# Performance work log

Hardware: AMD Instinct MI355X
Metric: run time of the kernel (lower is better)

Reference implementation:

```python
import jax, jax.numpy as jnp
import numpy as np

NHEAD = 8
TOPKS = (8, 8)  # topk per level, coarse -> fine


def _to_bshd(x):
    # [B, C, H, W] -> [B, H*W, nhead, d]  (matches rearrange 'b c h w -> b (h w) c' + view)
    b, c, h, w = x.shape
    return jnp.transpose(x.reshape(b, c, h * w), (0, 2, 1)).reshape(b, h * w, NHEAD, c // NHEAD)


def _coarse_level(q, k, v, topk):
    b, c, h, w = k.shape
    d = c // NHEAD
    q_, k_, v_ = _to_bshd(q), _to_bshd(k), _to_bshd(v)
    temp = 1.0 / (d ** 0.5)
    A = jax.nn.softmax(jnp.einsum('nlhd,nshd->nlsh', q_, k_) * temp, axis=2)  # [b,L,S,h]
    _, idx = jax.lax.top_k(jnp.swapaxes(A, 2, 3), topk)  # [b,L,h,k]
    idx = jnp.swapaxes(idx, 2, 3)                        # [b,L,k,h]
    msg = jnp.einsum('nlsh,nshd->nlhd', A, v_)           # [b,L,h,d]
    topk_pos = jnp.stack([idx // w, idx % w])            # [2,b,L,k,h]
    return msg, topk_pos


def _fine_level(q, k, v, topk_pos, topk_prev, topk):
    b, c, h0, w0 = q.shape
    w1 = k.shape[3]
    d = c // NHEAD
    k_, v_ = _to_bshd(k), _to_bshd(v)
    H2, W2 = h0 // 2, w0 // 2
    L0 = H2 * W2
    # query grouped into 2x2 quads: [b, L0, 4, h, d]
    q_ = q.reshape(b, c, H2, 2, W2, 2).transpose(0, 2, 4, 3, 5, 1).reshape(b, L0, 4, NHEAD, d)
    tp = topk_pos * 2  # coarse positions -> fine grid
    cand = [(tp[0] + x) * w1 + tp[1] + y for x in (0, 1) for y in (0, 1)]
    t2 = topk_prev * 4
    idx = jnp.stack(cand, axis=3).reshape(b, L0, t2, NHEAD)  # [b,L,t2,h]
    idx_bh = idx.transpose(0, 3, 1, 2).reshape(b, NHEAD, L0 * t2)

    def gather(p):  # p: [b,S,h,d] -> gathered [b,L,t2,h,d]
        g = jnp.take_along_axis(jnp.swapaxes(p, 1, 2), idx_bh[..., None], axis=2)
        return g.reshape(b, NHEAD, L0, t2, d).transpose(0, 2, 3, 1, 4)

    tk, tv = gather(k_), gather(v_)
    temp = 1.0 / (d ** 0.5)
    A = jax.nn.softmax(jnp.einsum('blqhd,blthd->blqth', q_, tk) * temp, axis=3)  # [b,L,4,t2,h]
    _, ti = jax.lax.top_k(jnp.moveaxis(A, 3, 4), topk)  # [b,L,4,h,k]
    ti = jnp.moveaxis(ti, 4, 3)                         # [b,L,4,k,h]
    msg = jnp.einsum('blqth,blthd->blqhd', A, tv)       # [b,L,4,h,d]
    idx_b = jnp.broadcast_to(idx[:, :, None], (b, L0, 4, t2, NHEAD))
    gidx = jnp.take_along_axis(idx_b, ti, axis=3)       # [b,L,4,k,h] flat fine-grid indices
    gidx = gidx.reshape(b, H2, W2, 2, 2, topk, NHEAD).transpose(0, 1, 3, 2, 4, 5, 6)
    gidx = gidx.reshape(b, h0 * w0, topk, NHEAD)
    return msg, gidx


def _forward(q_fine, q_coarse, k_fine, k_coarse, v_fine, v_coarse, weight):
    msg0, topk_pos = _coarse_level(q_coarse, k_coarse, v_coarse, TOPKS[0])
    msg1, _ = _fine_level(q_fine, k_fine, v_fine, topk_pos, TOPKS[0], TOPKS[1])
    w = jax.nn.softmax(weight, axis=0)
    fm = msg0 * w[0]                  # [b,Lc,h,d]
    fm = fm[:, :, None] + msg1 * w[1]  # [b,Lc,4,h,d]
    b, Hc, Wc = q_coarse.shape[0], q_coarse.shape[2], q_coarse.shape[3]
    d = fm.shape[-1]
    # rearrange 'b (H W) (t1 t2) h d -> b (H t1 W t2) h d'
    fm = fm.reshape(b, Hc, Wc, 2, 2, NHEAD, d).transpose(0, 1, 3, 2, 4, 5, 6)
    return fm.reshape(b, Hc * Wc * 4, NHEAD, d)


def setup_inputs() -> dict:
    key = jax.random.key(0)
    ks = jax.random.split(key, 7)
    B, C = 4, 128
    return {
        'q_fine': jax.random.normal(ks[0], (B, C, 64, 64), jnp.float32),
        'q_coarse': jax.random.normal(ks[1], (B, C, 32, 32), jnp.float32),
        'k_fine': jax.random.normal(ks[2], (B, C, 64, 64), jnp.float32),
        'k_coarse': jax.random.normal(ks[3], (B, C, 32, 32), jnp.float32),
        'v_fine': jax.random.normal(ks[4], (B, C, 64, 64), jnp.float32),
        'v_coarse': jax.random.normal(ks[5], (B, C, 32, 32), jnp.float32),
        'weight': jax.random.normal(ks[6], (2,), jnp.float32),
    }


def reference(q_fine, q_coarse, k_fine, k_coarse, v_fine, v_coarse, weight):
    return _forward(q_fine, q_coarse, k_fine, k_coarse, v_fine, v_coarse, weight)
```

## Files before the change

kernel.cpp:

```cpp
#include <hip/hip_runtime.h>
#include <stdint.h>

#define TEMP 0.25f

typedef unsigned short u16;
typedef short v8s __attribute__((ext_vector_type(8)));
typedef float v4f __attribute__((ext_vector_type(4)));

static __device__ __forceinline__ uint32_t f2b_bits(float f){
    union { float f; uint32_t i; } x; x.f = f;
    uint32_t u = x.i;
    return (u + 0x7FFFu + ((u >> 16) & 1u)) >> 16;
}
static __device__ __forceinline__ float b2f(u16 u){
    union { uint32_t i; float f; } x; x.i = ((uint32_t)u) << 16; return x.f;
}
static __device__ __forceinline__ float bl(uint32_t u){
    union { uint32_t i; float f; } x; x.i = u << 16; return x.f;
}
static __device__ __forceinline__ float bh(uint32_t u){
    union { uint32_t i; float f; } x; x.i = u & 0xffff0000u; return x.f;
}
static __device__ __forceinline__ uint4 pack8(const uint32_t* e){
    return make_uint4(e[0] | (e[1] << 16), e[2] | (e[3] << 16),
                      e[4] | (e[5] << 16), e[6] | (e[7] << 16));
}
union U8S { uint4 u; v8s s; };
union I4S { int i[4]; v8s s; };
static __device__ __forceinline__ v8s asv8s(uint4 u){ U8S x; x.u = u; return x.s; }
static __device__ __forceinline__ v8s swapq(v8s v){
    union { v8s s; int i[4]; } x; x.s = v;
    #pragma unroll
    for (int k = 0; k < 4; ++k) x.i[k] = __shfl_xor(x.i[k], 32);
    return x.s;
}

__global__ __launch_bounds__(256)
void pack_coarse(const float* __restrict__ kc, const float* __restrict__ vc,
                 uint4* __restrict__ KP1, uint4* __restrict__ KP3,
                 uint4* __restrict__ VP1)
{
    const int bh = blockIdx.x;
    const int kv = blockIdx.y;
    const int z  = blockIdx.z;
    const int b = bh >> 3, h = bh & 7;
    const int tid = threadIdx.x;
    const size_t sbase = (size_t)(b * 128 + h * 16) * 1024;
    const size_t fbase = (size_t)bh * 64 * 64;

    #pragma unroll
    for (int it = 0; it < 2; ++it){
        int task = it * 256 + tid;
        int kt = z * 8 + (task >> 6), ln = task & 63;
        int quad = ln >> 4, col = ln & 15;
        if (kv == 0){
            uint32_t e1[8], e3[8];
            #pragma unroll
            for (int j = 0; j < 8; ++j){
                int dch = (quad & 1) * 8 + j;
                float x = kc[sbase + (size_t)dch * 1024 + kt * 16 + col];
                uint32_t u0 = f2b_bits(x);
                float r1 = x - b2f((u16)u0);
                uint32_t u1 = f2b_bits(r1);
                float r2 = r1 - b2f((u16)u1);
                uint32_t u2 = f2b_bits(r2);
                e1[j] = (quad < 2) ? u0 : u1;
                e3[j] = (quad < 2) ? u2 : u0;
            }
            KP1[fbase + kt * 64 + ln] = pack8(e1);
            KP3[fbase + kt * 64 + ln] = pack8(e3);
        } else {
            uint32_t e[8];
            #pragma unroll
            for (int j = 0; j < 8; ++j){
                int key = kt * 16 + (quad & 1) * 8 + j;
                float x = vc[sbase + (size_t)col * 1024 + key];
                uint32_t u0 = f2b_bits(x);
                uint32_t u1 = f2b_bits(x - b2f((u16)u0));
                e[j] = (quad < 2) ? u0 : u1;
            }
            VP1[fbase + kt * 64 + ln] = pack8(e);
        }
    }
}

__global__ __launch_bounds__(256)
void coarse_mfma(const float* __restrict__ qc,
                 const uint4* __restrict__ KP1, const uint4* __restrict__ KP3,
                 const uint4* __restrict__ VP1,
                 float* __restrict__ msg0, int* __restrict__ topk_out)
{
    const int ltile = blockIdx.x;
    const int h = blockIdx.y, b = blockIdx.z;
    const int bh = b * 8 + h;
    const int tid = threadIdx.x, lane = tid & 63, wv = tid >> 6;
    const int quad = lane >> 4, col = lane & 15;
    const int lbase = ltile * 16;

    __shared__ uint32_t tls[4][16 * 20];
    __shared__ float rred[2][4][16];
    __shared__ float pvred[4][16][16];
    __shared__ float tkv[4][16][8];
    __shared__ int   tki[4][16][8];

    v8s a1, a3;
    {
        int row = lbase + col;
        int dch0 = (quad & 1) * 8;
        #pragma unroll
        for (int j = 0; j < 8; ++j){
            float x = qc[(size_t)(b * 128 + h * 16 + dch0 + j) * 1024 + row] * TEMP;
            uint32_t u0 = f2b_bits(x);
            float r1 = x - b2f((u16)u0);
            uint32_t u1 = f2b_bits(r1);
            float r2 = r1 - b2f((u16)u1);
            uint32_t u2 = f2b_bits(r2);
            a1[j] = (short)(quad < 2 ? u0 : u1);
            a3[j] = (short)(quad < 2 ? u0 : u2);
        }
    }

    const size_t fbase = (size_t)bh * 64 * 64;
    v4f sc[16];
    #pragma unroll
    for (int kt = 0; kt < 16; ++kt){
        int ktg = wv * 16 + kt;
        v8s b1 = asv8s(KP1[fbase + (size_t)ktg * 64 + lane]);
        v8s b3 = asv8s(KP3[fbase + (size_t)ktg * 64 + lane]);
        v8s b2 = swapq(b1);
        v4f c = {0.f, 0.f, 0.f, 0.f};
        c = __builtin_amdgcn_mfma_f32_16x16x32_bf16(a1, b1, c, 0, 0, 0);
        c = __builtin_amdgcn_mfma_f32_16x16x32_bf16(a1, b2, c, 0, 0, 0);
        c = __builtin_amdgcn_mfma_f32_16x16x32_bf16(a3, b3, c, 0, 0, 0);
        sc[kt] = c;
    }

    #pragma unroll
    for (int r = 0; r < 4; ++r){
        float m = sc[0][r];
        #pragma unroll
        for (int kt = 1; kt < 16; ++kt) m = fmaxf(m, sc[kt][r]);
        #pragma unroll
        for (int off = 1; off < 16; off <<= 1) m = fmaxf(m, __shfl_xor(m, off));
        if (col == 0) rred[0][wv][quad * 4 + r] = m;
    }
    __syncthreads();
    #pragma unroll
    for (int r = 0; r < 4; ++r){
        int row = quad * 4 + r;
        float m = fmaxf(fmaxf(rred[0][0][row], rred[0][1][row]),
                        fmaxf(rred[0][2][row], rred[0][3][row]));
        #pragma unroll
        for (int kt = 0; kt < 16; ++kt) sc[kt][r] = __expf(sc[kt][r] - m);
    }
    #pragma unroll
    for (int r = 0; r < 4; ++r){
        float s = 0.f;
        #pragma unroll
        for (int kt = 0; kt < 16; ++kt) s += sc[kt][r];
        #pragma unroll
        for (int off = 1; off < 16; off <<= 1) s += __shfl_xor(s, off);
        if (col == 0) rred[1][wv][quad * 4 + r] = s;
    }

    v4f acc = {0.f, 0.f, 0.f, 0.f};
    uint32_t* tw = tls[wv];
    const int rdbase = col * 20 + 8 * (quad & 1);
    const uint32_t selp = (quad < 2) ? 0x05040100u : 0x07060302u;
    #pragma unroll
    for (int kt = 0; kt < 16; ++kt){
        #pragma unroll
        for (int r = 0; r < 4; ++r){
            float x = sc[kt][r];
            uint32_t u0 = f2b_bits(x);
            uint32_t u1 = f2b_bits(x - b2f((u16)u0));
            tw[(quad * 4 + r) * 20 + col] = u0 | (u1 << 16);
        }
        __builtin_amdgcn_s_waitcnt(0xC07F);
        uint4 d0 = *(const uint4*)&tw[rdbase];
        uint4 d1 = *(const uint4*)&tw[rdbase + 4];
        I4S ux;
        ux.i[0] = __builtin_amdgcn_perm(d0.y, d0.x, selp);
        ux.i[1] = __builtin_amdgcn_perm(d0.w, d0.z, selp);
        ux.i[2] = __builtin_amdgcn_perm(d1.y, d1.x, selp);
        ux.i[3] = __builtin_amdgcn_perm(d1.w, d1.z, selp);
        v8s ap = ux.s;
        v8s bv1 = asv8s(VP1[fbase + (size_t)(wv * 16 + kt) * 64 + lane]);
        v8s bv2 = swapq(bv1);
        acc = __builtin_amdgcn_mfma_f32_16x16x32_bf16(ap, bv1, acc, 0, 0, 0);
        acc = __builtin_amdgcn_mfma_f32_16x16x32_bf16(ap, bv2, acc, 0, 0, 0);
    }
    #pragma unroll
    for (int r = 0; r < 4; ++r) pvred[wv][quad * 4 + r][col] = acc[r];

    #pragma unroll
    for (int r = 0; r < 4; ++r){
        int row = quad * 4 + r;
        #pragma unroll
        for (int rnd = 0; rnd < 8; ++rnd){
            float bv = sc[0][r]; int bk = 0;
            #pragma unroll
            for (int kt = 1; kt < 16; ++kt){
                bool g = sc[kt][r] > bv;
                bv = g ? sc[kt][r] : bv; bk = g ? kt : bk;
            }
            int bi = bk * 16 + col;
            #pragma unroll
            for (int off = 1; off < 16; off <<= 1){
                float ov = __shfl_xor(bv, off);
                int   oi = __shfl_xor(bi, off);
                bool g = (ov > bv) || (ov == bv && oi < bi);
                bv = g ? ov : bv; bi = g ? oi : bi;
            }
            if ((bi & 15) == col){
                int ktw = bi >> 4;
                #pragma unroll
                for (int kt = 0; kt < 16; ++kt)
                    if (kt == ktw) sc[kt][r] = -1.0f;
            }
            if (col == rnd){ tkv[wv][row][rnd] = bv; tki[wv][row][rnd] = wv * 256 + bi; }
        }
    }
    __syncthreads();

    {
        int row = tid >> 4, dd = tid & 15;
        float v = pvred[0][row][dd] + pvred[1][row][dd] +
                  pvred[2][row][dd] + pvred[3][row][dd];
        float s = rred[1][0][row] + rred[1][1][row] +
                  rred[1][2][row] + rred[1][3][row];
        msg0[((size_t)((b * 1024 + lbase + row) * 8 + h)) * 16 + dd] = v / s;
    }
    if (tid < 16){
        int row = tid;
        int* tp = topk_out + (((b * 1024 + lbase + row) * 8 + h) * 8);
        int p[4] = {0, 0, 0, 0};
        #pragma unroll
        for (int rnd = 0; rnd < 8; ++rnd){
            float bv = -3.0f; int bw = 0, bi = 0x7fffffff;
            #pragma unroll
            for (int w = 0; w < 4; ++w){
                float v = tkv[w][row][p[w]];
                int   i = tki[w][row][p[w]];
                bool g = (v > bv) || (v == bv && i < bi);
                bv = g ? v : bv; bi = g ? i : bi; bw = g ? w : bw;
            }
            tp[rnd] = bi;
            p[bw]++;
        }
    }
}

__global__ __launch_bounds__(512, 2)
void coarse_kernel(const float* __restrict__ qc, const float* __restrict__ kc,
                   const float* __restrict__ vc, float* __restrict__ msg0,
                   int* __restrict__ topk_out)
{
    const int ltile = blockIdx.x;
    const int h = blockIdx.y, b = blockIdx.z;
    const int tid = threadIdx.x;
    const int lane = tid & 63, wv = tid >> 6;
    const int lbase = ltile * 32;
    __shared__ float sKV[16 * 1024];
    const size_t base = (size_t)(b * 128 + h * 16) * 1024;
    {
        const float4* gK = (const float4*)(kc + base);
        float4* lK = (float4*)sKV;
        #pragma unroll
        for (int i = 0; i < 8; ++i) lK[tid + 512 * i] = gK[tid + 512 * i];
    }
    float qreg[4];
    {
        int dq = lane & 15;
        #pragma unroll
        for (int li = 0; li < 4; ++li){
            int l = lbase + wv * 4 + li;
            qreg[li] = qc[base + (size_t)dq * 1024 + l] * TEMP;
        }
    }
    __syncthreads();
    float p[4][16];
    #pragma unroll
    for (int li = 0; li < 4; ++li)
        #pragma unroll
        for (int j = 0; j < 16; ++j) p[li][j] = 0.f;
    #pragma unroll
    for (int dch = 0; dch < 16; ++dch){
        float kf[16];
        #pragma unroll
        for (int ch = 0; ch < 4; ++ch){
            float4 kv = *(const float4*)&sKV[dch * 1024 + ch * 256 + (lane << 2)];
            kf[ch*4+0] = kv.x; kf[ch*4+1] = kv.y; kf[ch*4+2] = kv.z; kf[ch*4+3] = kv.w;
        }
        float qs[4];
        #pragma unroll
        for (int li = 0; li < 4; ++li) qs[li] = __shfl(qreg[li], dch);
        #pragma unroll
        for (int li = 0; li < 4; ++li)
            #pragma unroll
            for (int j = 0; j < 16; ++j) p[li][j] = fmaf(qs[li], kf[j], p[li][j]);
    }
    float invs[4];
    #pragma unroll
    for (int li = 0; li < 4; ++li){
        float m = p[li][0];
        #pragma unroll
        for (int j = 1; j < 16; ++j) m = fmaxf(m, p[li][j]);
        #pragma unroll
        for (int off = 32; off > 0; off >>= 1) m = fmaxf(m, __shfl_xor(m, off));
        float s = 0.f;
        #pragma unroll
        for (int j = 0; j < 16; ++j){ p[li][j] = __expf(p[li][j] - m); s += p[li][j]; }
        #pragma unroll
        for (int off = 32; off > 0; off >>= 1) s += __shfl_xor(s, off);
        invs[li] = 1.0f / s;
    }
    __syncthreads();
    {
        const float4* gV = (const float4*)(vc + base);
        float4* lV = (float4*)sKV;
        #pragma unroll
        for (int i = 0; i < 8; ++i) lV[tid + 512 * i] = gV[tid + 512 * i];
    }
    __syncthreads();
    float outv = 0.f;
    #pragma unroll
    for (int dd = 0; dd < 16; ++dd){
        float vf[16];
        #pragma unroll
        for (int ch = 0; ch < 4; ++ch){
            float4 vv = *(const float4*)&sKV[dd * 1024 + ch * 256 + (lane << 2)];
            vf[ch*4+0] = vv.x; vf[ch*4+1] = vv.y; vf[ch*4+2] = vv.z; vf[ch*4+3] = vv.w;
        }
        float a[4];
        #pragma unroll
        for (int li = 0; li < 4; ++li){
            float s = 0.f;
            #pragma unroll
            for (int j = 0; j < 16; ++j) s = fmaf(p[li][j], vf[j], s);
            a[li] = s;
        }
        #pragma unroll
        for (int off = 32; off > 0; off >>= 1)
            #pragma unroll
            for (int li = 0; li < 4; ++li) a[li] += __shfl_xor(a[li], off);
        #pragma unroll
        for (int li = 0; li < 4; ++li)
            outv = (lane == li * 16 + dd) ? a[li] * invs[li] : outv;
    }
    {
        int li = lane >> 4, dd = lane & 15;
        int l = lbase + wv * 4 + li;
        msg0[(size_t)((b * 1024 + l) * 8 + h) * 16 + dd] = outv;
    }
    const int lanebase = lane << 4;
    int mytk = 0;
    for (int r = 0; r < 8; ++r){
        float bv[4]; int bi[4];
        #pragma unroll
        for (int li = 0; li < 4; ++li){
            float v0[8]; int j0[8];
            #pragma unroll
            for (int k = 0; k < 8; ++k){
                bool g = p[li][2*k+1] > p[li][2*k];
                v0[k] = g ? p[li][2*k+1] : p[li][2*k];
                j0[k] = g ? 2*k+1 : 2*k;
            }
            float v1[4]; int j1[4];
            #pragma unroll
            for (int k = 0; k < 4; ++k){
                bool g = v0[2*k+1] > v0[2*k];
                v1[k] = g ? v0[2*k+1] : v0[2*k];
                j1[k] = g ? j0[2*k+1] : j0[2*k];
            }
            float v2[2]; int j2[2];
            #pragma unroll
            for (int k = 0; k < 2; ++k){
                bool g = v1[2*k+1] > v1[2*k];
                v2[k] = g ? v1[2*k+1] : v1[2*k];
                j2[k] = g ? j1[2*k+1] : j1[2*k];
            }
            bool g3 = v2[1] > v2[0];
            bv[li] = g3 ? v2[1] : v2[0];
            bi[li] = lanebase | (g3 ? j2[1] : j2[0]);
        }
        #pragma unroll
        for (int off = 32; off > 0; off >>= 1){
            #pragma unroll
            for (int li = 0; li < 4; ++li){
                float ov = __shfl_xor(bv[li], off);
                int   oi = __shfl_xor(bi[li], off);
                bool g = (ov > bv[li]) || (ov == bv[li] && oi < bi[li]);
                bv[li] = g ? ov : bv[li];
                bi[li] = g ? oi : bi[li];
            }
        }
        #pragma unroll
        for (int li = 0; li < 4; ++li){
            #pragma unroll
            for (int j = 0; j < 16; ++j)
                p[li][j] = (bi[li] == (lanebase | j)) ? -1.0f : p[li][j];
            mytk = (lane == li * 8 + r) ? bi[li] : mytk;
        }
    }
    if (lane < 32){
        int li = lane >> 3, r = lane & 7;
        int jw = mytk & 15, lw = mytk >> 4;
        int s = ((jw >> 2) << 8) | (lw << 2) | (jw & 3);
        int l = lbase + wv * 4 + li;
        topk_out[((b * 1024 + l) * 8 + h) * 8 + r] = s;
    }
}

__global__ __launch_bounds__(256)
void pack_kernel(const float* __restrict__ kf, const float* __restrict__ vf,
                 const float* __restrict__ qf,
                 uint32_t* __restrict__ packed, float* __restrict__ qT)
{
    const int pt = blockIdx.x;
    const int b  = blockIdx.y;
    const int z  = blockIdx.z;
    const float* src = (z == 0) ? kf : (z == 1) ? vf : qf;
    const int tid = threadIdx.x;
    __shared__ float tile[64][129];
    const int pos0 = pt * 64;

    #pragma unroll
    for (int it = 0; it < 8; ++it){
        int task = it * 256 + tid;
        int ch = task >> 4, p4 = task & 15;
        float4 v = *(const float4*)(src + (size_t)(b * 128 + ch) * 4096 + pos0 + p4 * 4);
        tile[p4*4+0][ch] = v.x; tile[p4*4+1][ch] = v.y;
        tile[p4*4+2][ch] = v.z; tile[p4*4+3][ch] = v.w;
    }
    __syncthreads();

    if (z == 2){
        #pragma unroll
        for (int it = 0; it < 8; ++it){
            int task = it * 256 + tid;
            int p = task >> 5, c4 = task & 31;
            float4 v = make_float4(tile[p][c4*4+0], tile[p][c4*4+1],
                                   tile[p][c4*4+2], tile[p][c4*4+3]);
            *(float4*)(qT + ((size_t)(b * 4096) + pos0 + p) * 128 + c4 * 4) = v;
        }
    } else {
        const int x = pt;
        #pragma unroll
        for (int it = 0; it < 2; ++it){
            int task = it * 256 + tid;
            int h = task >> 6, y = task & 63;
            int pprime = ((x >> 1) * 32 + (y >> 1)) * 4 + (x & 1) * 2 + (y & 1);
            size_t line = (size_t)(b * 8 + h) * 4096 + pprime;
            uint32_t dw[8];
            #pragma unroll
            for (int i = 0; i < 8; ++i){
                uint32_t lo = f2b_bits(tile[y][h * 16 + 2 * i]);
                uint32_t hi = f2b_bits(tile[y][h * 16 + 2 * i + 1]);
                dw[i] = lo | (hi << 16);
            }
            uint4* dst4 = (uint4*)packed + line * 4 + z * 2;
            dst4[0] = make_uint4(dw[0], dw[1], dw[2], dw[3]);
            dst4[1] = make_uint4(dw[4], dw[5], dw[6], dw[7]);
        }
    }
}

__global__ __launch_bounds__(256)
void fine_kernel(const float* __restrict__ qf, const float* __restrict__ kf,
                 const float* __restrict__ vf,
                 const float* __restrict__ qTg, const uint32_t* __restrict__ packed,
                 int transposed,
                 const float* __restrict__ wt,
                 const int* __restrict__ topk_in, const float* __restrict__ msg0,
                 float* __restrict__ out)
{
    const int l0 = blockIdx.x;
    const int b  = blockIdx.y;
    const int tid = threadIdx.x;

    __shared__ float vT[8][16][34];
    __shared__ float qT[8][4][16];
    __shared__ float pT[8][4][32];
    __shared__ int tkS[8][8];

    if (tid < 64) tkS[tid >> 3][tid & 7] =
        topk_in[((b * 1024 + l0) * 8 + (tid >> 3)) * 8 + (tid & 7)];
    __syncthreads();

    const int i = l0 >> 5, j = l0 & 31;
    const int hh = tid >> 5;
    const int t  = tid & 31;
    const int kk = t >> 2, cp = t & 3;

    float k[16];
    {
        int s = tkS[hh][kk];
        if (transposed){
            const uint4* pk = (const uint4*)packed;
            size_t line = (size_t)(b * 8 + hh) * 4096 + s * 4 + cp;
            uint4 a0 = pk[line*4+0], a1 = pk[line*4+1];
            uint4 a2 = pk[line*4+2], a3 = pk[line*4+3];
            k[0]=bl(a0.x);  k[1]=bh(a0.x);  k[2]=bl(a0.y);  k[3]=bh(a0.y);
            k[4]=bl(a0.z);  k[5]=bh(a0.z);  k[6]=bl(a0.w);  k[7]=bh(a0.w);
            k[8]=bl(a1.x);  k[9]=bh(a1.x);  k[10]=bl(a1.y); k[11]=bh(a1.y);
            k[12]=bl(a1.z); k[13]=bh(a1.z); k[14]=bl(a1.w); k[15]=bh(a1.w);
            vT[hh][0][t]=bl(a2.x);  vT[hh][1][t]=bh(a2.x);
            vT[hh][2][t]=bl(a2.y);  vT[hh][3][t]=bh(a2.y);
            vT[hh][4][t]=bl(a2.z);  vT[hh][5][t]=bh(a2.z);
            vT[hh][6][t]=bl(a2.w);  vT[hh][7][t]=bh(a2.w);
            vT[hh][8][t]=bl(a3.x);  vT[hh][9][t]=bh(a3.x);
            vT[hh][10][t]=bl(a3.y); vT[hh][11][t]=bh(a3.y);
            vT[hh][12][t]=bl(a3.z); vT[hh][13][t]=bh(a3.z);
            vT[hh][14][t]=bl(a3.w); vT[hh][15][t]=bh(a3.w);
        } else {
            int pos = (2 * (s >> 5) + (cp >> 1)) * 64 + 2 * (s & 31) + (cp & 1);
            size_t gb = (size_t)(b * 128 + hh * 16) * 4096 + pos;
            #pragma unroll
            for (int ch = 0; ch < 16; ++ch){
                k[ch] = kf[gb + (size_t)ch * 4096];
                vT[hh][ch][t] = vf[gb + (size_t)ch * 4096];
            }
        }
    }
    if (tid < 128){
        int qh = tid >> 4, aq = (tid >> 2) & 3, c4 = tid & 3;
        int qpos = (2 * i + (aq >> 1)) * 64 + 2 * j + (aq & 1);
        if (transposed){
            float4 u = *(const float4*)(qTg + ((size_t)(b * 4096) + qpos) * 128 + qh * 16 + c4 * 4);
            qT[qh][aq][c4*4+0] = u.x * TEMP;
            qT[qh][aq][c4*4+1] = u.y * TEMP;
            qT[qh][aq][c4*4+2] = u.z * TEMP;
            qT[qh][aq][c4*4+3] = u.w * TEMP;
        } else {
            #pragma unroll
            for (int c = 0; c < 4; ++c)
                qT[qh][aq][c4*4+c] =
                    qf[(size_t)(b * 128 + qh * 16 + c4 * 4 + c) * 4096 + qpos] * TEMP;
        }
    }
    __syncthreads();

    {
        float sc[4] = {0.f, 0.f, 0.f, 0.f};
        #pragma unroll
        for (int dch = 0; dch < 16; ++dch){
            float kv = k[dch];
            #pragma unroll
            for (int q = 0; q < 4; ++q) sc[q] = fmaf(qT[hh][q][dch], kv, sc[q]);
        }
        #pragma unroll
        for (int q = 0; q < 4; ++q){
            float m = sc[q];
            #pragma unroll
            for (int off = 16; off > 0; off >>= 1) m = fmaxf(m, __shfl_xor(m, off, 32));
            float e = __expf(sc[q] - m);
            float s = e;
            #pragma unroll
            for (int off = 16; off > 0; off >>= 1) s += __shfl_xor(s, off, 32);
            pT[hh][q][t] = e / s;
        }
    }
    __syncthreads();

    {
        float w0 = wt[0], w1 = wt[1];
        float mx = fmaxf(w0, w1);
        float e0 = __expf(w0 - mx), e1 = __expf(w1 - mx);
        float w0f = e0 / (e0 + e1), w1f = e1 / (e0 + e1);

        int q0 = (tid >> 4) & 1;
        int dd = tid & 15;
        float a0 = 0.f, a1 = 0.f;
        #pragma unroll
        for (int tt = 0; tt < 16; ++tt){
            float v0 = vT[hh][dd][tt * 2], v1 = vT[hh][dd][tt * 2 + 1];
            float2 pA = *(const float2*)&pT[hh][q0][tt * 2];
            float2 pB = *(const float2*)&pT[hh][q0 + 2][tt * 2];
            a0 = fmaf(pA.x, v0, a0); a0 = fmaf(pA.y, v1, a0);
            a1 = fmaf(pB.x, v0, a1); a1 = fmaf(pB.y, v1, a1);
        }
        float m0 = msg0[(size_t)((b * 1024 + l0) * 8 + hh) * 16 + dd];
        float o0 = w0f * m0 + w1f * a0;
        float o1 = w0f * m0 + w1f * a1;
        int posA = (2 * i) * 64 + 2 * j + q0;
        int posB = (2 * i + 1) * 64 + 2 * j + q0;
        out[(size_t)((b * 4096 + posA) * 8 + hh) * 16 + dd] = o0;
        out[(size_t)((b * 4096 + posB) * 8 + hh) * 16 + dd] = o1;
    }
}

extern "C" void kernel_launch(void* const* d_in, const int* in_sizes, int n_in,
                              void* d_out, int out_size, void* d_ws, size_t ws_size,
                              hipStream_t stream)
{
    (void)in_sizes; (void)n_in; (void)out_size;

    const float* q_fine   = (const float*)d_in[0];
    const float* q_coarse = (const float*)d_in[1];
    const float* k_fine   = (const float*)d_in[2];
    const float* k_coarse = (const float*)d_in[3];
    const float* v_fine   = (const float*)d_in[4];
    const float* v_coarse = (const float*)d_in[5];
    const float* weight   = (const float*)d_in[6];

    const size_t MB = 1024 * 1024;
    float*    msg0   = (float*)d_ws;
    int*      topk   = (int*)((char*)d_ws + 2 * MB);
    float*    qT     = (float*)((char*)d_ws + 3 * MB);
    uint32_t* packed = (uint32_t*)((char*)d_ws + 11 * MB);
    uint4*    KP1    = (uint4*)((char*)d_ws + 19 * MB);
    uint4*    KP3    = (uint4*)((char*)d_ws + 21 * MB);
    uint4*    VP1    = (uint4*)((char*)d_ws + 23 * MB);
    const int doT = (ws_size >= 19 * MB) ? 1 : 0;
    const int doM = (ws_size >= 25 * MB) ? 1 : 0;

    if (doM){
        pack_coarse<<<dim3(32, 2, 8), dim3(256), 0, stream>>>(k_coarse, v_coarse,
                                                              KP1, KP3, VP1);
        coarse_mfma<<<dim3(64, 8, 4), dim3(256), 0, stream>>>(q_coarse, KP1, KP3, VP1,
                                                              msg0, topk);
    } else {
        coarse_kernel<<<dim3(32, 8, 4), dim3(512), 0, stream>>>(q_coarse, k_coarse,
                                                                v_coarse, msg0, topk);
    }

    if (doT){
        pack_kernel<<<dim3(64, 4, 3), dim3(256), 0, stream>>>(k_fine, v_fine, q_fine,
                                                              packed, qT);
    }

    fine_kernel<<<dim3(1024, 4), dim3(256), 0, stream>>>(q_fine, k_fine, v_fine,
                                                         qT, packed, doT,
                                                         weight, topk, msg0,
                                                         (float*)d_out);
}
```

Baseline: 218.1 us.

## Merge pack kernels into one launch and use DPP reductions in coarse kernel

Combines the fine-level packing and coarse-level packing into a single pack_all launch, removing one kernel launch and letting both pack jobs share the GPU at once. In coarse_mfma, the 16-lane shuffle reductions for max, sum and top-k argmax become DPP row operations, with the top-k using a packed 64-bit value/index key. The lane-32 swap via shuffles is replaced by a second global load at lane^32. Some bf16 hi-part conversions now truncate instead of rounding, which changes how the split-precision error is distributed between the high and low parts.

```diff
diff --git a/kernel.cpp b/kernel.cpp
--- a/kernel.cpp
+++ b/kernel.cpp
@@ -28,11 +28,34 @@
 union U8S { uint4 u; v8s s; };
 union I4S { int i[4]; v8s s; };
 static __device__ __forceinline__ v8s asv8s(uint4 u){ U8S x; x.u = u; return x.s; }
-static __device__ __forceinline__ v8s swapq(v8s v){
-    union { v8s s; int i[4]; } x; x.s = v;
-    #pragma unroll
-    for (int k = 0; k < 4; ++k) x.i[k] = __shfl_xor(x.i[k], 32);
-    return x.s;
+
+template<int C>
+static __device__ __forceinline__ float dppf(float x){
+    int xi = __float_as_int(x);
+    return __int_as_float(__builtin_amdgcn_update_dpp(xi, xi, C, 0xf, 0xf, false));
+}
+static __device__ __forceinline__ float red16_max(float m){
+    m = fmaxf(m, dppf<0xB1>(m));  m = fmaxf(m, dppf<0x4E>(m));
+    m = fmaxf(m, dppf<0x141>(m)); m = fmaxf(m, dppf<0x140>(m));
+    return m;
+}
+static __device__ __forceinline__ float red16_sum(float s){
+    s += dppf<0xB1>(s);  s += dppf<0x4E>(s);
+    s += dppf<0x141>(s); s += dppf<0x140>(s);
+    return s;
+}
+template<int C>
+static __device__ __forceinline__ uint64_t dppmax64(uint64_t k){
+    int hi = (int)(uint32_t)(k >> 32), lo = (int)(uint32_t)k;
+    uint32_t oh = (uint32_t)__builtin_amdgcn_update_dpp(hi, hi, C, 0xf, 0xf, false);
+    uint32_t ol = (uint32_t)__builtin_amdgcn_update_dpp(lo, lo, C, 0xf, 0xf, false);
+    uint64_t ok = ((uint64_t)oh << 32) | ol;
+    return ok > k ? ok : k;
+}
+static __device__ __forceinline__ uint64_t red16_maxkey(uint64_t k){
+    k = dppmax64<0xB1>(k);  k = dppmax64<0x4E>(k);
+    k = dppmax64<0x141>(k); k = dppmax64<0x140>(k);
+    return k;
 }
 
 __global__ __launch_bounds__(256)
@@ -85,6 +108,107 @@
 }
 
 __global__ __launch_bounds__(256)
+void pack_all(const float* __restrict__ kf, const float* __restrict__ vf,
+              const float* __restrict__ qf,
+              const float* __restrict__ kc, const float* __restrict__ vc,
+              uint32_t* __restrict__ packed, float* __restrict__ qT,
+              uint4* __restrict__ KP1, uint4* __restrict__ KP3,
+              uint4* __restrict__ VP1)
+{
+    __shared__ float tile[64][129];
+    const int bid = blockIdx.x;
+    const int tid = threadIdx.x;
+
+    if (bid < 768){
+        const int pt = bid & 63, b = (bid >> 6) & 3, z = bid >> 8;
+        const float* src = (z == 0) ? kf : (z == 1) ? vf : qf;
+        const int pos0 = pt * 64;
+
+        #pragma unroll
+        for (int it = 0; it < 8; ++it){
+            int task = it * 256 + tid;
+            int ch = task >> 4, p4 = task & 15;
+            float4 v = *(const float4*)(src + (size_t)(b * 128 + ch) * 4096 + pos0 + p4 * 4);
+            tile[p4*4+0][ch] = v.x; tile[p4*4+1][ch] = v.y;
+            tile[p4*4+2][ch] = v.z; tile[p4*4+3][ch] = v.w;
+        }
+        __syncthreads();
+
+        if (z == 2){
+            #pragma unroll
+            for (int it = 0; it < 8; ++it){
+                int task = it * 256 + tid;
+                int p = task >> 5, c4 = task & 31;
+                float4 v = make_float4(tile[p][c4*4+0], tile[p][c4*4+1],
+                                       tile[p][c4*4+2], tile[p][c4*4+3]);
+                *(float4*)(qT + ((size_t)(b * 4096) + pos0 + p) * 128 + c4 * 4) = v;
+            }
+        } else {
+            const int x = pt;
+            #pragma unroll
+            for (int it = 0; it < 2; ++it){
+                int task = it * 256 + tid;
+                int hq = task >> 6, y = task & 63;
+                int pprime = ((x >> 1) * 32 + (y >> 1)) * 4 + (x & 1) * 2 + (y & 1);
+                size_t line = (size_t)(b * 8 + hq) * 4096 + pprime;
+                uint32_t dw[8];
+                #pragma unroll
+                for (int i = 0; i < 8; ++i){
+                    uint32_t lo = f2b_bits(tile[y][hq * 16 + 2 * i]);
+                    uint32_t hi = f2b_bits(tile[y][hq * 16 + 2 * i + 1]);
+                    dw[i] = lo | (hi << 16);
+                }
+                uint4* dst4 = (uint4*)packed + line * 4 + z * 2;
+                dst4[0] = make_uint4(dw[0], dw[1], dw[2], dw[3]);
+                dst4[1] = make_uint4(dw[4], dw[5], dw[6], dw[7]);
+            }
+        }
+    } else {
+        const int f2 = bid - 768;
+        const int bh = f2 & 31, kv = (f2 >> 5) & 1, z = f2 >> 6;
+        const int b = bh >> 3, h = bh & 7;
+        const size_t sbase = (size_t)(b * 128 + h * 16) * 1024;
+        const size_t fbase = (size_t)bh * 64 * 64;
+
+        #pragma unroll
+        for (int it = 0; it < 2; ++it){
+            int task = it * 256 + tid;
+            int kt = z * 8 + (task >> 6), ln = task & 63;
+            int quad = ln >> 4, col = ln & 15;
+            if (kv == 0){
+                uint32_t e1[8], e3[8];
+                #pragma unroll
+                for (int j = 0; j < 8; ++j){
+                    int dch = (quad & 1) * 8 + j;
+                    float x = kc[sbase + (size_t)dch * 1024 + kt * 16 + col];
+                    uint32_t u0 = f2b_bits(x);
+                    float r1 = x - b2f((u16)u0);
+                    uint32_t u1 = f2b_bits(r1);
+                    float r2 = r1 - b2f((u16)u1);
+                    uint32_t u2 = f2b_bits(r2);
+                    e1[j] = (quad < 2) ? u0 : u1;
+                    e3[j] = (quad < 2) ? u2 : u0;
+                }
+                KP1[fbase + kt * 64 + ln] = pack8(e1);
+                KP3[fbase + kt * 64 + ln] = pack8(e3);
+            } else {
+                uint32_t e[8];
+                #pragma unroll
+                for (int j = 0; j < 8; ++j){
+                    int key = kt * 16 + (quad & 1) * 8 + j;
+                    float x = vc[sbase + (size_t)col * 1024 + key];
+                    uint32_t xb = __float_as_uint(x);
+                    uint32_t u0 = xb >> 16;
+                    uint32_t u1 = f2b_bits(x - b2f((u16)u0));
+                    e[j] = (quad < 2) ? u0 : u1;
+                }
+                VP1[fbase + kt * 64 + ln] = pack8(e);
+            }
+        }
+    }
+}
+
+__global__ __launch_bounds__(256)
 void coarse_mfma(const float* __restrict__ qc,
                  const uint4* __restrict__ KP1, const uint4* __restrict__ KP3,
                  const uint4* __restrict__ VP1,
@@ -95,6 +219,7 @@
     const int bh = b * 8 + h;
     const int tid = threadIdx.x, lane = tid & 63, wv = tid >> 6;
     const int quad = lane >> 4, col = lane & 15;
+    const int lanex = lane ^ 32;
     const int lbase = ltile * 16;
 
     __shared__ uint32_t tls[4][16 * 20];
@@ -126,8 +251,8 @@
     for (int kt = 0; kt < 16; ++kt){
         int ktg = wv * 16 + kt;
         v8s b1 = asv8s(KP1[fbase + (size_t)ktg * 64 + lane]);
+        v8s b2 = asv8s(KP1[fbase + (size_t)ktg * 64 + lanex]);
         v8s b3 = asv8s(KP3[fbase + (size_t)ktg * 64 + lane]);
-        v8s b2 = swapq(b1);
         v4f c = {0.f, 0.f, 0.f, 0.f};
         c = __builtin_amdgcn_mfma_f32_16x16x32_bf16(a1, b1, c, 0, 0, 0);
         c = __builtin_amdgcn_mfma_f32_16x16x32_bf16(a1, b2, c, 0, 0, 0);
@@ -140,8 +265,7 @@
         float m = sc[0][r];
         #pragma unroll
         for (int kt = 1; kt < 16; ++kt) m = fmaxf(m, sc[kt][r]);
-        #pragma unroll
-        for (int off = 1; off < 16; off <<= 1) m = fmaxf(m, __shfl_xor(m, off));
+        m = red16_max(m);
         if (col == 0) rred[0][wv][quad * 4 + r] = m;
     }
     __syncthreads();
@@ -158,8 +282,7 @@
         float s = 0.f;
         #pragma unroll
         for (int kt = 0; kt < 16; ++kt) s += sc[kt][r];
-        #pragma unroll
-        for (int off = 1; off < 16; off <<= 1) s += __shfl_xor(s, off);
+        s = red16_sum(s);
         if (col == 0) rred[1][wv][quad * 4 + r] = s;
     }
 
@@ -172,7 +295,7 @@
         #pragma unroll
         for (int r = 0; r < 4; ++r){
             float x = sc[kt][r];
-            uint32_t u0 = f2b_bits(x);
+            uint32_t u0 = __float_as_uint(x) >> 16;
             uint32_t u1 = f2b_bits(x - b2f((u16)u0));
             tw[(quad * 4 + r) * 20 + col] = u0 | (u1 << 16);
         }
@@ -186,7 +309,7 @@
         ux.i[3] = __builtin_amdgcn_perm(d1.w, d1.z, selp);
         v8s ap = ux.s;
         v8s bv1 = asv8s(VP1[fbase + (size_t)(wv * 16 + kt) * 64 + lane]);
-        v8s bv2 = swapq(bv1);
+        v8s bv2 = asv8s(VP1[fbase + (size_t)(wv * 16 + kt) * 64 + lanex]);
         acc = __builtin_amdgcn_mfma_f32_16x16x32_bf16(ap, bv1, acc, 0, 0, 0);
         acc = __builtin_amdgcn_mfma_f32_16x16x32_bf16(ap, bv2, acc, 0, 0, 0);
     }
@@ -205,13 +328,11 @@
                 bv = g ? sc[kt][r] : bv; bk = g ? kt : bk;
             }
             int bi = bk * 16 + col;
-            #pragma unroll
-            for (int off = 1; off < 16; off <<= 1){
-                float ov = __shfl_xor(bv, off);
-                int   oi = __shfl_xor(bi, off);
-                bool g = (ov > bv) || (ov == bv && oi < bi);
-                bv = g ? ov : bv; bi = g ? oi : bi;
-            }
+            uint64_t k = ((uint64_t)(uint32_t)__float_as_int(bv) << 32)
+                       | (uint32_t)(~bi);
+            k = red16_maxkey(k);
+            bv = __int_as_float((int)(uint32_t)(k >> 32));
+            bi = (int)(~(uint32_t)k);
             if ((bi & 15) == col){
                 int ktw = bi >> 4;
                 #pragma unroll
@@ -615,19 +736,26 @@
     const int doT = (ws_size >= 19 * MB) ? 1 : 0;
     const int doM = (ws_size >= 25 * MB) ? 1 : 0;
 
-    if (doM){
-        pack_coarse<<<dim3(32, 2, 8), dim3(256), 0, stream>>>(k_coarse, v_coarse,
-                                                              KP1, KP3, VP1);
+    if (doM && doT){
+        pack_all<<<dim3(1280), dim3(256), 0, stream>>>(k_fine, v_fine, q_fine,
+                                                       k_coarse, v_coarse,
+                                                       packed, qT, KP1, KP3, VP1);
         coarse_mfma<<<dim3(64, 8, 4), dim3(256), 0, stream>>>(q_coarse, KP1, KP3, VP1,
                                                               msg0, topk);
     } else {
-        coarse_kernel<<<dim3(32, 8, 4), dim3(512), 0, stream>>>(q_coarse, k_coarse,
-                                                                v_coarse, msg0, topk);
-    }
-
-    if (doT){
-        pack_kernel<<<dim3(64, 4, 3), dim3(256), 0, stream>>>(k_fine, v_fine, q_fine,
-                                                              packed, qT);
+        if (doM){
+            pack_coarse<<<dim3(32, 2, 8), dim3(256), 0, stream>>>(k_coarse, v_coarse,
+                                                                  KP1, KP3, VP1);
+            coarse_mfma<<<dim3(64, 8, 4), dim3(256), 0, stream>>>(q_coarse, KP1, KP3, VP1,
+                                                                  msg0, topk);
+        } else {
+            coarse_kernel<<<dim3(32, 8, 4), dim3(512), 0, stream>>>(q_coarse, k_coarse,
+                                                                    v_coarse, msg0, topk);
+        }
+        if (doT){
+            pack_kernel<<<dim3(64, 4, 3), dim3(256), 0, stream>>>(k_fine, v_fine, q_fine,
+                                                                  packed, qT);
+        }
     }
 
     fine_kernel<<<dim3(1024, 4), dim3(256), 0, stream>>>(q_fine, k_fine, v_fine,
```

Result: faster. 196.4 us (-9.9%).
